# Kernel optimization log

Measured on AMD Instinct MI355X. Metric: run time of the kernel, lower is better.

The kernel has to match this reference:

```python
import jax, jax.numpy as jnp
import numpy as np

HEADS = 6
G = 4  # redundant group repeat factor in the original module
EPS = 1e-5


def _dw_bn(x, w, gamma, beta, mean, var):
    # depthwise 3x3 conv (stride 1, pad 1, no bias) + BatchNorm (eval mode)
    C = x.shape[1]
    y = jax.lax.conv_general_dilated(
        x, w, window_strides=(1, 1), padding=[(1, 1), (1, 1)],
        dimension_numbers=('NCHW', 'OIHW', 'NCHW'), feature_group_count=C)
    inv = gamma / jnp.sqrt(var + EPS)
    return y * inv[None, :, None, None] + (beta - mean * inv)[None, :, None, None]


def setup_inputs() -> dict:
    key = jax.random.key(0)
    ks = jax.random.split(key, 20)
    B, Cin, Cout, H, W = 8, 192, 192, 28, 28
    inp = {
        'x': jax.random.normal(ks[0], (B, H * W, Cin), jnp.float32),
        'h': H, 'w': W,
    }
    s = 0.1
    for i, p in enumerate(['q', 'k', 'v']):
        inp[f'dw{p}_w'] = jax.random.normal(ks[1 + i], (Cin, 1, 3, 3), jnp.float32) * s
        bk = jax.random.split(ks[4 + i], 4)
        inp[f'bn{p}_g'] = 1.0 + 0.1 * jax.random.normal(bk[0], (Cin,), jnp.float32)
        inp[f'bn{p}_b'] = 0.1 * jax.random.normal(bk[1], (Cin,), jnp.float32)
        inp[f'bn{p}_m'] = 0.1 * jax.random.normal(bk[2], (Cin,), jnp.float32)
        inp[f'bn{p}_v'] = jax.random.uniform(bk[3], (Cin,), jnp.float32, 0.5, 1.5)
        inp[f'p{p}_w'] = jax.random.normal(ks[7 + i], (Cout, Cin), jnp.float32) * (Cin ** -0.5)
        inp[f'p{p}_b'] = 0.01 * jax.random.normal(ks[10 + i], (Cout,), jnp.float32)
    inp['po_w'] = jax.random.normal(ks[13], (Cout, Cout), jnp.float32) * (Cout ** -0.5)
    inp['po_b'] = 0.01 * jax.random.normal(ks[14], (Cout,), jnp.float32)
    return inp


def reference(x, h, w,
              dwq_w, bnq_g, bnq_b, bnq_m, bnq_v, pq_w, pq_b,
              dwk_w, bnk_g, bnk_b, bnk_m, bnk_v, pk_w, pk_b,
              dwv_w, bnv_g, bnv_b, bnv_m, bnv_v, pv_w, pv_b,
              po_w, po_b):
    B, N, Cin = x.shape
    Cout = pq_w.shape[0]
    ch = Cout // HEADS  # per-head channel dim
    x4 = jnp.transpose(x, (0, 2, 1)).reshape(B, Cin, h, w)

    q = _dw_bn(x4, dwq_w, bnq_g, bnq_b, bnq_m, bnq_v)
    k = _dw_bn(x4, dwk_w, bnk_g, bnk_b, bnk_m, bnk_v)
    v = _dw_bn(x4, dwv_w, bnv_g, bnv_b, bnv_m, bnv_v)

    # 1x1 conv projections
    q = jnp.einsum('oc,bcij->boij', pq_w, q) + pq_b[None, :, None, None]
    k = jnp.einsum('oc,bcij->boij', pk_w, k) + pk_b[None, :, None, None]
    v = jnp.einsum('oc,bcij->boij', pv_w, v) + pv_b[None, :, None, None]

    # split heads: channels are (head, ch) ordered -> (B, heads, ch, h, w)
    qh = q.reshape(B, HEADS, ch, h, w)
    kh = k.reshape(B, HEADS, ch, h, w)
    vh = v.reshape(B, HEADS, ch, h, w)

    scale = Cout ** -0.5  # NOTE: original scales by dim_out**-0.5, not head_dim
    score = jnp.einsum('bhcij,bhckl->bhijkl', qh, kh) * scale
    attn = jax.nn.softmax(score.reshape(B, HEADS, h, w, h * w), axis=-1)
    attn = attn.reshape(B, HEADS, h, w, h, w)

    out = jnp.einsum('bhijkl,bhckl->bhcij', attn, vh)  # (B, heads, ch, h, w)
    # original output channel order is (ch, heads) via 'b c h g i j -> b (c h) g i j'
    out = jnp.transpose(out, (0, 2, 1, 3, 4))  # (B, ch, heads, h, w)
    out = jnp.broadcast_to(out[:, :, :, None], (B, ch, HEADS, G, h, w))
    out = out.reshape(B, ch * HEADS, G, h, w)

    y = jnp.einsum('oc,bcgij->bogij', po_w, out) + po_b[None, :, None, None, None]
    return y
```

## Files before the change

kernel.cpp:

```cpp
#include <hip/hip_runtime.h>
#include <math.h>

namespace {
constexpr int kB = 8;
constexpr int kC = 192;
constexpr int kH = 28;
constexpr int kW = 28;
constexpr int kN = 784;
constexpr int kHEADS = 6;
constexpr int kG = 4;
constexpr float kEPS = 1e-5f;
constexpr float kQS = 0.07216878364870322f * 1.4426950408889634f;
constexpr int kNP = 800;
}

typedef __attribute__((ext_vector_type(8))) short bf16x8;
typedef __attribute__((ext_vector_type(4))) float f32x4;

union VU { ushort4 hlf[2]; bf16x8 v; };

static __device__ __forceinline__ unsigned short f2bf(float f) {
    union { float f; unsigned int u; } v; v.f = f;
    unsigned int r = v.u + 0x7fffu + ((v.u >> 16) & 1u);
    return (unsigned short)(r >> 16);
}

static __device__ __forceinline__ float fexp2(float x) {
    return __builtin_amdgcn_exp2f(x);
}

__global__ __launch_bounds__(256) void prep_kernel(
    const float* __restrict__ pqw, const float* __restrict__ pkw,
    const float* __restrict__ pvw, const float* __restrict__ pow_,
    const float* __restrict__ dwq, const float* __restrict__ dwk,
    const float* __restrict__ dwv,
    unsigned short* __restrict__ Wq, unsigned short* __restrict__ Wk,
    unsigned short* __restrict__ Wv, unsigned short* __restrict__ Wo,
    float* __restrict__ dwT)
{
    const int aux = blockIdx.x * 256 + threadIdx.x;
    if (aux < 36864) {
        const int e0 = aux * 4;
        const int mat = e0 / (kC * kC);
        const int r = e0 % (kC * kC);
        if (mat < 3) {
            const float* src = (mat == 0) ? pqw : (mat == 1) ? pkw : pvw;
            unsigned short* dst = (mat == 0) ? Wq : (mat == 1) ? Wk : Wv;
            const f32x4 v = *(const f32x4*)&src[r];
            ushort4 p;
            p.x = f2bf(v[0]); p.y = f2bf(v[1]); p.z = f2bf(v[2]); p.w = f2bf(v[3]);
            *(ushort4*)&dst[r] = p;
        } else {
            const int o = r / kC, c0 = r % kC;
            ushort4 p;
            unsigned short* pp = &p.x;
#pragma unroll
            for (int e = 0; e < 4; ++e) {
                const int c = c0 + e;
                pp[e] = f2bf(pow_[o * kC + (c & 31) * kHEADS + (c >> 5)]);
            }
            *(ushort4*)&Wo[o * kC + c0] = p;
        }
    } else {
        const int r = aux - 36864;
        if (r < 3 * 9 * kC) {
            const int br = r / (9 * kC);
            const int rem = r % (9 * kC);
            const int tap = rem / kC, c = rem % kC;
            const float* dw = (br == 0) ? dwq : (br == 1) ? dwk : dwv;
            dwT[r] = dw[c * 9 + tap];
        }
    }
}

__global__ __launch_bounds__(768, 6) void dwproj_kernel(
    const float* __restrict__ x,
    const float* __restrict__ gq, const float* __restrict__ bq,
    const float* __restrict__ mq, const float* __restrict__ vq,
    const float* __restrict__ gk, const float* __restrict__ bk,
    const float* __restrict__ mk, const float* __restrict__ vk,
    const float* __restrict__ gv, const float* __restrict__ bv,
    const float* __restrict__ mv, const float* __restrict__ vv,
    const float* __restrict__ dwT,
    const unsigned short* __restrict__ Wq, const unsigned short* __restrict__ Wk,
    const unsigned short* __restrict__ Wv,
    const float* __restrict__ pqb, const float* __restrict__ pkb,
    const float* __restrict__ pvb,
    unsigned short* __restrict__ Qb, unsigned short* __restrict__ Kb,
    unsigned short* __restrict__ Vb)
{
    __shared__ unsigned short Xs[3][16][200];

    const int b  = blockIdx.x & 7;
    const int n0 = (blockIdx.x >> 3) * 16;
    const int t = threadIdx.x;
    const int w = t >> 6, l = t & 63, q16 = l & 15, u = l >> 4;

    bf16x8 wp0, wp1, wp2, wp3, wp4, wp5;
    {
        const int unit0 = w * 3;
        const int br0 = unit0 / 12;
        const int ob0 = (unit0 % 12) * 16;
        const unsigned short* W0 = (br0 == 0) ? Wq : (br0 == 1) ? Wk : Wv;
        const unsigned short* Wr0 = W0 + (size_t)(ob0 + q16) * kC + u * 8;
        wp0 = *(const bf16x8*)(Wr0 + 0 * 32);
        wp1 = *(const bf16x8*)(Wr0 + 1 * 32);
        wp2 = *(const bf16x8*)(Wr0 + 2 * 32);
        wp3 = *(const bf16x8*)(Wr0 + 3 * 32);
        wp4 = *(const bf16x8*)(Wr0 + 4 * 32);
        wp5 = *(const bf16x8*)(Wr0 + 5 * 32);
    }

    {
        const int cg = t % 48;
        const int c0 = cg * 4;
        const int pos = t / 48;
        const int n = n0 + pos;
        const int i = n / kW, j = n % kW;

        f32x4 aq = {0.f, 0.f, 0.f, 0.f};
        f32x4 ak = {0.f, 0.f, 0.f, 0.f};
        f32x4 av = {0.f, 0.f, 0.f, 0.f};
        const float* xb = x + (size_t)b * kN * kC + c0;
#pragma unroll
        for (int di = -1; di <= 1; ++di) {
            const int ii = i + di;
            if (ii < 0 || ii >= kH) continue;
#pragma unroll
            for (int dj = -1; dj <= 1; ++dj) {
                const int jj = j + dj;
                if (jj < 0 || jj >= kW) continue;
                const int tap = (di + 1) * 3 + (dj + 1);
                const f32x4 xv = *(const f32x4*)&xb[(size_t)(ii * kW + jj) * kC];
                const f32x4 wq4 = *(const f32x4*)&dwT[(0 * 9 + tap) * kC + c0];
                const f32x4 wk4 = *(const f32x4*)&dwT[(1 * 9 + tap) * kC + c0];
                const f32x4 wv4 = *(const f32x4*)&dwT[(2 * 9 + tap) * kC + c0];
                aq += xv * wq4;
                ak += xv * wk4;
                av += xv * wv4;
            }
        }
        const f32x4 g0 = *(const f32x4*)&gq[c0], b0 = *(const f32x4*)&bq[c0];
        const f32x4 m0 = *(const f32x4*)&mq[c0], v0 = *(const f32x4*)&vq[c0];
        const f32x4 g1 = *(const f32x4*)&gk[c0], b1 = *(const f32x4*)&bk[c0];
        const f32x4 m1 = *(const f32x4*)&mk[c0], v1 = *(const f32x4*)&vk[c0];
        const f32x4 g2 = *(const f32x4*)&gv[c0], b2 = *(const f32x4*)&bv[c0];
        const f32x4 m2 = *(const f32x4*)&mv[c0], v2 = *(const f32x4*)&vv[c0];
        ushort4 pq, pk, pv;
        unsigned short* qq = &pq.x;
        unsigned short* qk = &pk.x;
        unsigned short* qv = &pv.x;
#pragma unroll
        for (int e = 0; e < 4; ++e) {
            const float iq = g0[e] * rsqrtf(v0[e] + kEPS);
            const float ik = g1[e] * rsqrtf(v1[e] + kEPS);
            const float iv = g2[e] * rsqrtf(v2[e] + kEPS);
            qq[e] = f2bf(aq[e] * iq + (b0[e] - m0[e] * iq));
            qk[e] = f2bf(ak[e] * ik + (b1[e] - m1[e] * ik));
            qv[e] = f2bf(av[e] * iv + (b2[e] - m2[e] * iv));
        }
        *(ushort4*)&Xs[0][pos][c0] = pq;
        *(ushort4*)&Xs[1][pos][c0] = pk;
        *(ushort4*)&Xs[2][pos][c0] = pv;
    }
    __syncthreads();

#pragma unroll
    for (int k3 = 0; k3 < 3; ++k3) {
        const int unit = w * 3 + k3;
        const int br = unit / 12;
        const int ob = (unit % 12) * 16;
        const unsigned short* W = (br == 0) ? Wq : (br == 1) ? Wk : Wv;
        const float* bias       = (br == 0) ? pqb : (br == 1) ? pkb : pvb;

        f32x4 acc = {0.f, 0.f, 0.f, 0.f};
        const unsigned short* Wr = W + (size_t)(ob + q16) * kC + u * 8;
#pragma unroll
        for (int kk = 0; kk < 6; ++kk) {
            const bf16x8 wa = (k3 == 0)
                ? (kk == 0 ? wp0 : kk == 1 ? wp1 : kk == 2 ? wp2
                   : kk == 3 ? wp3 : kk == 4 ? wp4 : wp5)
                : *(const bf16x8*)(Wr + kk * 32);
            const bf16x8 xa = *(const bf16x8*)&Xs[br][q16][u * 8 + kk * 32];
            acc = __builtin_amdgcn_mfma_f32_16x16x32_bf16(wa, xa, acc, 0, 0, 0);
        }
        const int hh = ob >> 5;
        const int ch0 = (ob & 31) + 4 * u;
        const f32x4 bi = *(const f32x4*)&bias[ob + 4 * u];
        const int n = n0 + q16;
        if (br < 2) {
            const float sc = (br == 0) ? kQS : 1.0f;
            ushort4 p;
            p.x = f2bf((acc[0] + bi[0]) * sc);
            p.y = f2bf((acc[1] + bi[1]) * sc);
            p.z = f2bf((acc[2] + bi[2]) * sc);
            p.w = f2bf((acc[3] + bi[3]) * sc);
            unsigned short* dst = ((br == 0) ? Qb : Kb) +
                ((size_t)(b * kHEADS + hh) * kNP + n) * 32 + ch0;
            *(ushort4*)dst = p;
        } else {
            unsigned short* dst = Vb +
                ((size_t)(b * kHEADS + hh) * 32 + ch0) * kNP + n;
            dst[0 * kNP] = f2bf(acc[0] + bi[0]);
            dst[1 * kNP] = f2bf(acc[1] + bi[1]);
            dst[2 * kNP] = f2bf(acc[2] + bi[2]);
            dst[3 * kNP] = f2bf(acc[3] + bi[3]);
        }
    }
}

__global__ __launch_bounds__(768, 6) void attnout_kernel(
    const unsigned short* __restrict__ Qbf, const unsigned short* __restrict__ Kbf,
    const unsigned short* __restrict__ Vbf, const unsigned short* __restrict__ Wo,
    const float* __restrict__ pob, float* __restrict__ Y)
{
    __shared__ unsigned short AOs[16][200];
    __shared__ float Mrg[6][64][9];

    const int b  = blockIdx.x & 7;
    const int i0 = (blockIdx.x >> 3) * 16;
    const int t = threadIdx.x;
    const int w = t >> 6;
    const int h = w % 6;
    const int s = w / 6;
    const int l = t & 63;
    const int q16 = l & 15;
    const int u = l >> 4;

    const unsigned short* Qp = Qbf + ((size_t)(b * kHEADS + h) * kNP + i0) * 32;
    const unsigned short* Kp = Kbf + (size_t)(b * kHEADS + h) * kNP * 32;
    const unsigned short* Vr0 = Vbf + ((size_t)(b * kHEADS + h) * 32 + q16) * kNP;
    const unsigned short* Vr1 = Vr0 + (size_t)16 * kNP;

    const bf16x8 qa = *(const bf16x8*)(Qp + q16 * 32 + u * 8);

    f32x4 oa0 = {0.f, 0.f, 0.f, 0.f};
    f32x4 oa1 = {0.f, 0.f, 0.f, 0.f};
    f32x4 la  = {0.f, 0.f, 0.f, 0.f};
    f32x4 lb  = {0.f, 0.f, 0.f, 0.f};

    const int tile_begin = s ? 12 : 0;
    const int tile_end   = s ? 24 : 12;

    bf16x8 kc0 = *(const bf16x8*)(Kp + (size_t)(tile_begin * 32 + q16) * 32 + u * 8);
    bf16x8 kc1 = *(const bf16x8*)(Kp + (size_t)(tile_begin * 32 + 16 + q16) * 32 + u * 8);
    bf16x8 kn0, kn1;

    for (int tile = tile_begin; tile < tile_end; ++tile) {
        const int t0 = tile * 32;
        if (tile + 1 < tile_end) {
            const int t1 = t0 + 32;
            kn0 = *(const bf16x8*)(Kp + (size_t)(t1 + q16) * 32 + u * 8);
            kn1 = *(const bf16x8*)(Kp + (size_t)(t1 + 16 + q16) * 32 + u * 8);
        }
        VU v0, v1;
        v0.hlf[0] = *(const ushort4*)(Vr0 + t0 + 4 * u);
        v0.hlf[1] = *(const ushort4*)(Vr0 + t0 + 16 + 4 * u);
        v1.hlf[0] = *(const ushort4*)(Vr1 + t0 + 4 * u);
        v1.hlf[1] = *(const ushort4*)(Vr1 + t0 + 16 + 4 * u);
        __builtin_amdgcn_s_setprio(1);
        f32x4 d0 = {0.f, 0.f, 0.f, 0.f};
        f32x4 d1 = {0.f, 0.f, 0.f, 0.f};
        d0 = __builtin_amdgcn_mfma_f32_16x16x32_bf16(kc0, qa, d0, 0, 0, 0);
        d1 = __builtin_amdgcn_mfma_f32_16x16x32_bf16(kc1, qa, d1, 0, 0, 0);
        f32x4 ve0, ve1;
        ve0[0] = fexp2(d0[0]); ve0[1] = fexp2(d0[1]);
        ve0[2] = fexp2(d0[2]); ve0[3] = fexp2(d0[3]);
        ve1[0] = fexp2(d1[0]); ve1[1] = fexp2(d1[1]);
        ve1[2] = fexp2(d1[2]); ve1[3] = fexp2(d1[3]);
        la += ve0; lb += ve1;
        union { unsigned int wd[4]; bf16x8 v; } pa;
        asm("v_cvt_pk_bf16_f32 %0, %1, %2" : "=v"(pa.wd[0]) : "v"(ve0[0]), "v"(ve0[1]));
        asm("v_cvt_pk_bf16_f32 %0, %1, %2" : "=v"(pa.wd[1]) : "v"(ve0[2]), "v"(ve0[3]));
        asm("v_cvt_pk_bf16_f32 %0, %1, %2" : "=v"(pa.wd[2]) : "v"(ve1[0]), "v"(ve1[1]));
        asm("v_cvt_pk_bf16_f32 %0, %1, %2" : "=v"(pa.wd[3]) : "v"(ve1[2]), "v"(ve1[3]));
        oa0 = __builtin_amdgcn_mfma_f32_16x16x32_bf16(pa.v, v0.v, oa0, 0, 0, 0);
        oa1 = __builtin_amdgcn_mfma_f32_16x16x32_bf16(pa.v, v1.v, oa1, 0, 0, 0);
        __builtin_amdgcn_s_setprio(0);
        kc0 = kn0; kc1 = kn1;
    }
    if (s) {
        const int t0 = 768;
        const bf16x8 ka0 = *(const bf16x8*)(Kp + (size_t)(t0 + q16) * 32 + u * 8);
        VU v0, v1;
        const ushort4 z4 = {0, 0, 0, 0};
        v0.hlf[0] = *(const ushort4*)(Vr0 + t0 + 4 * u);
        v0.hlf[1] = z4;
        v1.hlf[0] = *(const ushort4*)(Vr1 + t0 + 4 * u);
        v1.hlf[1] = z4;
        f32x4 d0 = {0.f, 0.f, 0.f, 0.f};
        d0 = __builtin_amdgcn_mfma_f32_16x16x32_bf16(ka0, qa, d0, 0, 0, 0);
        f32x4 ve0;
        ve0[0] = fexp2(d0[0]); ve0[1] = fexp2(d0[1]);
        ve0[2] = fexp2(d0[2]); ve0[3] = fexp2(d0[3]);
        la += ve0;
        union { unsigned int wd[4]; bf16x8 v; } pa;
        asm("v_cvt_pk_bf16_f32 %0, %1, %2" : "=v"(pa.wd[0]) : "v"(ve0[0]), "v"(ve0[1]));
        asm("v_cvt_pk_bf16_f32 %0, %1, %2" : "=v"(pa.wd[1]) : "v"(ve0[2]), "v"(ve0[3]));
        pa.wd[2] = 0u;
        pa.wd[3] = 0u;
        oa0 = __builtin_amdgcn_mfma_f32_16x16x32_bf16(pa.v, v0.v, oa0, 0, 0, 0);
        oa1 = __builtin_amdgcn_mfma_f32_16x16x32_bf16(pa.v, v1.v, oa1, 0, 0, 0);
    }
    float psum = ((la[0] + la[1]) + (la[2] + la[3])) +
                 ((lb[0] + lb[1]) + (lb[2] + lb[3]));

    if (s == 1) {
        float* Mp = Mrg[h][l];
        Mp[0] = oa0[0]; Mp[1] = oa0[1]; Mp[2] = oa0[2]; Mp[3] = oa0[3];
        Mp[4] = oa1[0]; Mp[5] = oa1[1]; Mp[6] = oa1[2]; Mp[7] = oa1[3];
        Mp[8] = psum;
    }
    __syncthreads();
    if (s == 0) {
        const float* Mp = Mrg[h][l];
        oa0[0] += Mp[0]; oa0[1] += Mp[1]; oa0[2] += Mp[2]; oa0[3] += Mp[3];
        oa1[0] += Mp[4]; oa1[1] += Mp[5]; oa1[2] += Mp[6]; oa1[3] += Mp[7];
        float lsum = psum + Mp[8];
        lsum += __shfl_xor(lsum, 16);
        lsum += __shfl_xor(lsum, 32);
        const float rinv = 1.0f / lsum;
        const float r0 = __shfl(rinv, u * 4 + 0);
        const float r1 = __shfl(rinv, u * 4 + 1);
        const float r2 = __shfl(rinv, u * 4 + 2);
        const float r3 = __shfl(rinv, u * 4 + 3);
        AOs[4 * u + 0][h * 32 + q16] = f2bf(oa0[0] * r0);
        AOs[4 * u + 1][h * 32 + q16] = f2bf(oa0[1] * r1);
        AOs[4 * u + 2][h * 32 + q16] = f2bf(oa0[2] * r2);
        AOs[4 * u + 3][h * 32 + q16] = f2bf(oa0[3] * r3);
        AOs[4 * u + 0][h * 32 + 16 + q16] = f2bf(oa1[0] * r0);
        AOs[4 * u + 1][h * 32 + 16 + q16] = f2bf(oa1[1] * r1);
        AOs[4 * u + 2][h * 32 + 16 + q16] = f2bf(oa1[2] * r2);
        AOs[4 * u + 3][h * 32 + 16 + q16] = f2bf(oa1[3] * r3);
    }
    __syncthreads();

    {
        const int ob = w * 16;
        f32x4 acc = {0.f, 0.f, 0.f, 0.f};
        const unsigned short* Wr = Wo + (size_t)(ob + q16) * kC + u * 8;
#pragma unroll
        for (int kk = 0; kk < 6; ++kk) {
            const bf16x8 wa = *(const bf16x8*)(Wr + kk * 32);
            const bf16x8 xa = *(const bf16x8*)&AOs[q16][u * 8 + kk * 32];
            acc = __builtin_amdgcn_mfma_f32_16x16x32_bf16(wa, xa, acc, 0, 0, 0);
        }
        const f32x4 bi = *(const f32x4*)&pob[ob + 4 * u];
        const int n = i0 + q16;
#pragma unroll
        for (int r = 0; r < 4; ++r) {
            const int o = ob + 4 * u + r;
            const float val = acc[r] + bi[r];
            float* yp = Y + (((size_t)b * kC + o) * kG) * kN + n;
            yp[0 * kN] = val;
            yp[1 * kN] = val;
            yp[2 * kN] = val;
            yp[3 * kN] = val;
        }
    }
}

extern "C" void kernel_launch(void* const* d_in, const int* in_sizes, int n_in,
                              void* d_out, int out_size, void* d_ws, size_t ws_size,
                              hipStream_t stream) {
    const float* x     = (const float*)d_in[0];
    const float* dwq_w = (const float*)d_in[3];
    const float* bnq_g = (const float*)d_in[4];
    const float* bnq_b = (const float*)d_in[5];
    const float* bnq_m = (const float*)d_in[6];
    const float* bnq_v = (const float*)d_in[7];
    const float* pq_w  = (const float*)d_in[8];
    const float* pq_b  = (const float*)d_in[9];
    const float* dwk_w = (const float*)d_in[10];
    const float* bnk_g = (const float*)d_in[11];
    const float* bnk_b = (const float*)d_in[12];
    const float* bnk_m = (const float*)d_in[13];
    const float* bnk_v = (const float*)d_in[14];
    const float* pk_w  = (const float*)d_in[15];
    const float* pk_b  = (const float*)d_in[16];
    const float* dwv_w = (const float*)d_in[17];
    const float* bnv_g = (const float*)d_in[18];
    const float* bnv_b = (const float*)d_in[19];
    const float* bnv_m = (const float*)d_in[20];
    const float* bnv_v = (const float*)d_in[21];
    const float* pv_w  = (const float*)d_in[22];
    const float* pv_b  = (const float*)d_in[23];
    const float* po_w  = (const float*)d_in[24];
    const float* po_b  = (const float*)d_in[25];

    unsigned short* ws = (unsigned short*)d_ws;
    const size_t QSZ = (size_t)kB * kHEADS * kNP * 32;
    unsigned short* Qb = ws;
    unsigned short* Kb = Qb + QSZ;
    unsigned short* Vb = Kb + QSZ;
    unsigned short* Wq = Vb + QSZ;
    unsigned short* Wk = Wq + kC * kC;
    unsigned short* Wv = Wk + kC * kC;
    unsigned short* Wo = Wv + kC * kC;
    float* dwT = (float*)(Wo + kC * kC);

    prep_kernel<<<dim3(165), dim3(256), 0, stream>>>(
        pq_w, pk_w, pv_w, po_w, dwq_w, dwk_w, dwv_w,
        Wq, Wk, Wv, Wo, dwT);

    dwproj_kernel<<<dim3(kB * 49), dim3(768), 0, stream>>>(
        x,
        bnq_g, bnq_b, bnq_m, bnq_v,
        bnk_g, bnk_b, bnk_m, bnk_v,
        bnv_g, bnv_b, bnv_m, bnv_v,
        dwT, Wq, Wk, Wv, pq_b, pk_b, pv_b, Qb, Kb, Vb);

    attnout_kernel<<<dim3(kB * 49), dim3(768), 0, stream>>>(
        Qb, Kb, Vb, Wo, po_b, (float*)d_out);
}
```

Baseline: 66.55 us.

## Give each wave a full key sweep over two query tiles per block

The attention kernel no longer splits the key range between two wave groups that merge partial sums through shared memory. Each block now handles two 16-query tiles, and each wave processes all keys for one head and one query tile, so the merge buffer and one barrier disappear. The grid shrinks from 392 to 200 blocks, and the last tile is partly out of range and is masked. This trades fewer reductions and syncs for less parallelism and a longer serial loop per wave.

```diff
diff --git a/kernel.cpp b/kernel.cpp
--- a/kernel.cpp
+++ b/kernel.cpp
@@ -214,15 +214,16 @@
     const unsigned short* __restrict__ Vbf, const unsigned short* __restrict__ Wo,
     const float* __restrict__ pob, float* __restrict__ Y)
 {
-    __shared__ unsigned short AOs[16][200];
-    __shared__ float Mrg[6][64][9];
-
-    const int b  = blockIdx.x & 7;
-    const int i0 = (blockIdx.x >> 3) * 16;
+    __shared__ unsigned short AOs[2][16][200];
+
+    const int b    = blockIdx.x & 7;
+    const int base = (blockIdx.x >> 3) * 32;
     const int t = threadIdx.x;
     const int w = t >> 6;
-    const int h = w % 6;
-    const int s = w / 6;
+    const int h  = w % 6;
+    const int qs = w / 6;
+    const int i0 = base + qs * 16;
+    const bool valid = (i0 < kN);
     const int l = t & 63;
     const int q16 = l & 15;
     const int u = l >> 4;
@@ -239,16 +240,13 @@
     f32x4 la  = {0.f, 0.f, 0.f, 0.f};
     f32x4 lb  = {0.f, 0.f, 0.f, 0.f};
 
-    const int tile_begin = s ? 12 : 0;
-    const int tile_end   = s ? 24 : 12;
-
-    bf16x8 kc0 = *(const bf16x8*)(Kp + (size_t)(tile_begin * 32 + q16) * 32 + u * 8);
-    bf16x8 kc1 = *(const bf16x8*)(Kp + (size_t)(tile_begin * 32 + 16 + q16) * 32 + u * 8);
+    bf16x8 kc0 = *(const bf16x8*)(Kp + (size_t)(0 + q16) * 32 + u * 8);
+    bf16x8 kc1 = *(const bf16x8*)(Kp + (size_t)(16 + q16) * 32 + u * 8);
     bf16x8 kn0, kn1;
 
-    for (int tile = tile_begin; tile < tile_end; ++tile) {
+    for (int tile = 0; tile < 24; ++tile) {
         const int t0 = tile * 32;
-        if (tile + 1 < tile_end) {
+        if (tile + 1 < 24) {
             const int t1 = t0 + 32;
             kn0 = *(const bf16x8*)(Kp + (size_t)(t1 + q16) * 32 + u * 8);
             kn1 = *(const bf16x8*)(Kp + (size_t)(t1 + 16 + q16) * 32 + u * 8);
@@ -279,7 +277,7 @@
         __builtin_amdgcn_s_setprio(0);
         kc0 = kn0; kc1 = kn1;
     }
-    if (s) {
+    {
         const int t0 = 768;
         const bf16x8 ka0 = *(const bf16x8*)(Kp + (size_t)(t0 + q16) * 32 + u * 8);
         VU v0, v1;
@@ -302,60 +300,53 @@
         oa0 = __builtin_amdgcn_mfma_f32_16x16x32_bf16(pa.v, v0.v, oa0, 0, 0, 0);
         oa1 = __builtin_amdgcn_mfma_f32_16x16x32_bf16(pa.v, v1.v, oa1, 0, 0, 0);
     }
-    float psum = ((la[0] + la[1]) + (la[2] + la[3])) +
+    float lsum = ((la[0] + la[1]) + (la[2] + la[3])) +
                  ((lb[0] + lb[1]) + (lb[2] + lb[3]));
-
-    if (s == 1) {
-        float* Mp = Mrg[h][l];
-        Mp[0] = oa0[0]; Mp[1] = oa0[1]; Mp[2] = oa0[2]; Mp[3] = oa0[3];
-        Mp[4] = oa1[0]; Mp[5] = oa1[1]; Mp[6] = oa1[2]; Mp[7] = oa1[3];
-        Mp[8] = psum;
+    lsum += __shfl_xor(lsum, 16);
+    lsum += __shfl_xor(lsum, 32);
+    const float rinv = 1.0f / lsum;
+    const float r0 = __shfl(rinv, u * 4 + 0);
+    const float r1 = __shfl(rinv, u * 4 + 1);
+    const float r2 = __shfl(rinv, u * 4 + 2);
+    const float r3 = __shfl(rinv, u * 4 + 3);
+    if (valid) {
+        AOs[qs][4 * u + 0][h * 32 + q16] = f2bf(oa0[0] * r0);
+        AOs[qs][4 * u + 1][h * 32 + q16] = f2bf(oa0[1] * r1);
+        AOs[qs][4 * u + 2][h * 32 + q16] = f2bf(oa0[2] * r2);
+        AOs[qs][4 * u + 3][h * 32 + q16] = f2bf(oa0[3] * r3);
+        AOs[qs][4 * u + 0][h * 32 + 16 + q16] = f2bf(oa1[0] * r0);
+        AOs[qs][4 * u + 1][h * 32 + 16 + q16] = f2bf(oa1[1] * r1);
+        AOs[qs][4 * u + 2][h * 32 + 16 + q16] = f2bf(oa1[2] * r2);
+        AOs[qs][4 * u + 3][h * 32 + 16 + q16] = f2bf(oa1[3] * r3);
     }
     __syncthreads();
-    if (s == 0) {
-        const float* Mp = Mrg[h][l];
-        oa0[0] += Mp[0]; oa0[1] += Mp[1]; oa0[2] += Mp[2]; oa0[3] += Mp[3];
-        oa1[0] += Mp[4]; oa1[1] += Mp[5]; oa1[2] += Mp[6]; oa1[3] += Mp[7];
-        float lsum = psum + Mp[8];
-        lsum += __shfl_xor(lsum, 16);
-        lsum += __shfl_xor(lsum, 32);
-        const float rinv = 1.0f / lsum;
-        const float r0 = __shfl(rinv, u * 4 + 0);
-        const float r1 = __shfl(rinv, u * 4 + 1);
-        const float r2 = __shfl(rinv, u * 4 + 2);
-        const float r3 = __shfl(rinv, u * 4 + 3);
-        AOs[4 * u + 0][h * 32 + q16] = f2bf(oa0[0] * r0);
-        AOs[4 * u + 1][h * 32 + q16] = f2bf(oa0[1] * r1);
-        AOs[4 * u + 2][h * 32 + q16] = f2bf(oa0[2] * r2);
-        AOs[4 * u + 3][h * 32 + q16] = f2bf(oa0[3] * r3);
-        AOs[4 * u + 0][h * 32 + 16 + q16] = f2bf(oa1[0] * r0);
-        AOs[4 * u + 1][h * 32 + 16 + q16] = f2bf(oa1[1] * r1);
-        AOs[4 * u + 2][h * 32 + 16 + q16] = f2bf(oa1[2] * r2);
-        AOs[4 * u + 3][h * 32 + 16 + q16] = f2bf(oa1[3] * r3);
-    }
-    __syncthreads();
-
-    {
-        const int ob = w * 16;
+
+#pragma unroll
+    for (int k2 = 0; k2 < 2; ++k2) {
+        const int unit = w * 2 + k2;
+        const int qsel = unit / 12;
+        const int ob = (unit % 12) * 16;
         f32x4 acc = {0.f, 0.f, 0.f, 0.f};
         const unsigned short* Wr = Wo + (size_t)(ob + q16) * kC + u * 8;
 #pragma unroll
         for (int kk = 0; kk < 6; ++kk) {
             const bf16x8 wa = *(const bf16x8*)(Wr + kk * 32);
-            const bf16x8 xa = *(const bf16x8*)&AOs[q16][u * 8 + kk * 32];
+            const bf16x8 xa = *(const bf16x8*)&AOs[qsel][q16][u * 8 + kk * 32];
             acc = __builtin_amdgcn_mfma_f32_16x16x32_bf16(wa, xa, acc, 0, 0, 0);
         }
-        const f32x4 bi = *(const f32x4*)&pob[ob + 4 * u];
-        const int n = i0 + q16;
-#pragma unroll
-        for (int r = 0; r < 4; ++r) {
-            const int o = ob + 4 * u + r;
-            const float val = acc[r] + bi[r];
-            float* yp = Y + (((size_t)b * kC + o) * kG) * kN + n;
-            yp[0 * kN] = val;
-            yp[1 * kN] = val;
-            yp[2 * kN] = val;
-            yp[3 * kN] = val;
+        const int n = base + qsel * 16 + q16;
+        if (n < kN) {
+            const f32x4 bi = *(const f32x4*)&pob[ob + 4 * u];
+#pragma unroll
+            for (int r = 0; r < 4; ++r) {
+                const int o = ob + 4 * u + r;
+                const float val = acc[r] + bi[r];
+                float* yp = Y + (((size_t)b * kC + o) * kG) * kN + n;
+                yp[0 * kN] = val;
+                yp[1 * kN] = val;
+                yp[2 * kN] = val;
+                yp[3 * kN] = val;
+            }
         }
     }
 }
@@ -410,6 +401,6 @@
         bnv_g, bnv_b, bnv_m, bnv_v,
         dwT, Wq, Wk, Wv, pq_b, pk_b, pv_b, Qb, Kb, Vb);
 
-    attnout_kernel<<<dim3(kB * 49), dim3(768), 0, stream>>>(
+    attnout_kernel<<<dim3(kB * 25), dim3(768), 0, stream>>>(
         Qb, Kb, Vb, Wo, po_b, (float*)d_out);
 }
```

After: 67.54 us. No clear change (+1.5%).
